# Kernel optimization log

Hardware: AMD Instinct MI355X
Metric: run time of the kernel (lower is better)

Reference implementation:

```python
import jax, jax.numpy as jnp
import numpy as np

B = 262144      # points per batch
DIM = 3         # input_dim
L = 16          # levels
T = 19          # log2 hash table size
F = 2           # features per level
N_MIN, N_MAX = 16, 512

_b = np.exp((np.log(N_MAX) - np.log(N_MIN)) / (L - 1))
RES = np.floor(N_MIN * _b ** np.arange(L)).astype(np.float32).reshape(1, 1, L, 1)

# voxel corner offsets [1, DIM, 1, 2^DIM]
_border = np.empty((DIM, 2 ** DIM), dtype=np.uint32)
for i in range(DIM):
    _border[i, :] = np.array(([0] * 2 ** i + [1] * 2 ** i) * 2 ** (DIM - i - 1), dtype=np.uint32)
BORDER = _border.reshape(1, DIM, 1, 2 ** DIM)

# tiny-cuda-nn hash primes; all fit in uint32. Since the torch code takes the
# result mod 2^T (a power of two), int64 and uint32 arithmetic agree on the
# low bits, so uint32 hashing is bit-exact with the original.
PRIMES = np.array([1, 2654435761, 805459861], dtype=np.uint32)
MASK = np.uint32(2 ** T - 1)


def setup_inputs() -> dict:
    key = jax.random.key(0)
    k1, k2 = jax.random.split(key)
    x = jax.random.uniform(k1, (B, DIM), dtype=jnp.float32)  # coords in [0,1)
    tables = jax.random.uniform(k2, (L, 2 ** T, F), dtype=jnp.float32,
                                minval=-1e-4, maxval=1e-4)
    return {"x": x, "tables": tables}


def reference(x, tables):
    res = jnp.asarray(RES)                                   # [1,1,L,1]
    border = jnp.asarray(BORDER)                             # [1,DIM,1,2^DIM]
    primes = jnp.asarray(PRIMES)
    scaled = x[:, :, None, None] * res                       # [B,DIM,L,1]
    grid = jnp.floor(scaled).astype(jnp.uint32) + border     # [B,DIM,L,2^DIM]
    # spatial hash: xor of per-dim coord * prime, mod 2^T
    h = (grid[:, 0] * primes[0]) ^ (grid[:, 1] * primes[1]) ^ (grid[:, 2] * primes[2])
    idx = (h & MASK).astype(jnp.int32)                       # [B,L,2^DIM]
    gathered = tables[jnp.arange(L)[None, :, None], idx]     # [B,L,2^DIM,F]
    # multilinear interpolation weights
    w = jnp.prod(1.0 - jnp.abs(scaled - grid.astype(scaled.dtype)), axis=1)  # [B,L,2^DIM]
    out = jnp.einsum('blv,blvf->blf', w, gathered)           # [B,L,F]
    return out.reshape(x.shape[0], L * F)
```

## Files before the change

kernel.cpp:

```cpp
#include <hip/hip_runtime.h>


#define NB 262144
#define NL 16
#define TSIZE (1u << 19)
#define TMASK ((1u << 19) - 1u)
#define P1 2654435761u
#define P2 805459861u

#define NCL 3
#define CPTS 8192
#define COARSE_BLOCKS 256
#define CLDS_ENT (17 * 17 * 17)

#define E3 33
#define E4 41
#define E5 51
#define E6 65
#define DOFF3 0
#define DOFF4 35944
#define DOFF5 104872
#define DOFF6 237528
#define DENSE_TOTAL 512160

#define FC1 18513
#define FC2 53814
#define FC3 121440
#define FTOTAL 260865

#define FINE_TOTAL 6656
#define FINE_MAXPX 1024
#define GRID_BLOCKS (COARSE_BLOCKS + 8 * FINE_MAXPX)

typedef float vf2 __attribute__((ext_vector_type(2)));
typedef float vf4 __attribute__((ext_vector_type(4)));
typedef vf4 vf4a8 __attribute__((aligned(8), may_alias));
typedef float vf3 __attribute__((ext_vector_type(3)));
typedef vf3 vf3a4 __attribute__((aligned(4), may_alias));

__constant__ float RES_C[NL] = {16.f, 20.f, 25.f, 32.f, 40.f, 50.f, 64.f, 80.f,
                                101.f, 128.f, 161.f, 203.f, 256.f, 322.f, 406.f, 512.f};

__constant__ int XSPLIT[9] = {0, 1024, 2048, 2816, 3584, 4352, 5120, 5888, 6656};

__device__ __forceinline__ vf3 load_xyz(const float* __restrict__ p) {
  return *(const vf3a4*)p;
}

__device__ __forceinline__ void ngp_point_level(
    float px, float py, float pz, int l, const float* __restrict__ tables,
    float& o0, float& o1) {
  const float res = RES_C[l];
  const float sx = px * res, sy = py * res, sz = pz * res;
  const float fx = floorf(sx), fy = floorf(sy), fz = floorf(sz);
  const unsigned ix = (unsigned)fx, iy = (unsigned)fy, iz = (unsigned)fz;

  const unsigned hy0 = iy * P1, hy1 = hy0 + P1;
  const unsigned hz0 = iz * P2, hz1 = hz0 + P2;

  const float wx0 = 1.0f - fabsf(sx - fx);
  const float wx1 = 1.0f - fabsf(sx - (fx + 1.0f));
  const float wy0 = 1.0f - fabsf(sy - fy);
  const float wy1 = 1.0f - fabsf(sy - (fy + 1.0f));
  const float wz0 = 1.0f - fabsf(sz - fz);
  const float wz1 = 1.0f - fabsf(sz - (fz + 1.0f));

  const vf2* __restrict__ tbl2 = (const vf2*)tables + (size_t)l * TSIZE;
  const vf4* __restrict__ tbl4 = (const vf4*)tables + (size_t)l * (TSIZE / 2);

  unsigned hyz[4];
  hyz[0] = hy0 ^ hz0;
  hyz[1] = hy1 ^ hz0;
  hyz[2] = hy0 ^ hz1;
  hyz[3] = hy1 ^ hz1;

  vf2 g[8];
  if ((ix & 1u) == 0u) {
#pragma unroll
    for (int p = 0; p < 4; ++p) {
      const unsigned i0 = (ix ^ hyz[p]) & TMASK;
      const vf4 q = tbl4[i0 >> 1];
      vf2 lo; lo.x = q.x; lo.y = q.y;
      vf2 hi; hi.x = q.z; hi.y = q.w;
      const bool x0_is_lo = (i0 & 1u) == 0u;
      g[2 * p + 0] = x0_is_lo ? lo : hi;
      g[2 * p + 1] = x0_is_lo ? hi : lo;
    }
  } else {
#pragma unroll
    for (int p = 0; p < 4; ++p) {
      const unsigned i0 = (ix ^ hyz[p]) & TMASK;
      const unsigned i1 = ((ix + 1u) ^ hyz[p]) & TMASK;
      g[2 * p + 0] = tbl2[i0];
      g[2 * p + 1] = tbl2[i1];
    }
  }

  o0 = 0.0f; o1 = 0.0f;
#pragma unroll
  for (int v = 0; v < 8; ++v) {
    const float w = ((v & 1) ? wx1 : wx0) * ((v & 2) ? wy1 : wy0) * ((v & 4) ? wz1 : wz0);
    o0 = fmaf(w, g[v].x, o0);
    o1 = fmaf(w, g[v].y, o1);
  }
}

template <int E, int DOFF_>
__device__ __forceinline__ void dense_point(
    float px, float py, float pz, float res, const vf2* __restrict__ dense,
    float& o0, float& o1) {
  const float sx = px * res, sy = py * res, sz = pz * res;
  const float fx = floorf(sx), fy = floorf(sy), fz = floorf(sz);
  const int ix = (int)fx, iy = (int)fy, iz = (int)fz;

  const float wx0 = 1.0f - fabsf(sx - fx);
  const float wx1 = 1.0f - fabsf(sx - (fx + 1.0f));
  const float wy0 = 1.0f - fabsf(sy - fy);
  const float wy1 = 1.0f - fabsf(sy - (fy + 1.0f));
  const float wz0 = 1.0f - fabsf(sz - fz);
  const float wz1 = 1.0f - fabsf(sz - (fz + 1.0f));

  const vf2* __restrict__ dp = dense + DOFF_ + ix + E * iy + E * E * iz;

  vf2 g[8];
#pragma unroll
  for (int p = 0; p < 4; ++p) {
    const int row = ((p & 1) ? E : 0) + ((p & 2) ? E * E : 0);
    const vf4 q = *(const vf4a8*)(dp + row);
    g[2 * p + 0].x = q.x; g[2 * p + 0].y = q.y;
    g[2 * p + 1].x = q.z; g[2 * p + 1].y = q.w;
  }

  o0 = 0.0f; o1 = 0.0f;
#pragma unroll
  for (int v = 0; v < 8; ++v) {
    const float w = ((v & 1) ? wx1 : wx0) * ((v & 2) ? wy1 : wy0) * ((v & 4) ? wz1 : wz0);
    o0 = fmaf(w, g[v].x, o0);
    o1 = fmaf(w, g[v].y, o1);
  }
}

template <int E, int PLANES>
__device__ __forceinline__ void coarse_slab(
    const int lvl, const int zbase, const int c_lo, const int c_hi,
    const int cchunk, const float* __restrict__ x,
    const float* __restrict__ tables, vf2* __restrict__ ws,
    vf2* __restrict__ cache) {
  const int tid = threadIdx.x;
  const vf4* __restrict__ tbl4 = (const vf4*)tables + (size_t)lvl * (TSIZE / 2);

  constexpr int HE = (E + 1) / 2;
  constexpr int U = HE * E * PLANES;

  for (int u = tid; u < U; u += 512) {
    const int zp = u / (HE * E);
    const int rem = u - zp * (HE * E);
    const int iy = rem / HE;
    const int ixh = rem - iy * HE;
    const unsigned ix = 2u * (unsigned)ixh;
    const unsigned iz = (unsigned)(zbase + zp);
    const unsigned h0 = (ix ^ ((unsigned)iy * P1) ^ (iz * P2)) & TMASK;
    const vf4 q = tbl4[h0 >> 1];
    vf2 lo; lo.x = q.x; lo.y = q.y;
    vf2 hi; hi.x = q.z; hi.y = q.w;
    const bool x0_is_lo = (h0 & 1u) == 0u;
    const int d0 = (int)ix + E * iy + E * E * zp;
    cache[d0] = x0_is_lo ? lo : hi;
    if ((int)ix + 1 < E) cache[d0 + 1] = x0_is_lo ? hi : lo;
  }
  __syncthreads();

  const float res = RES_C[lvl];
  const int base = cchunk * CPTS;
#pragma unroll
  for (int k = 0; k < CPTS / 512; ++k) {
    const int b = base + k * 512 + tid;
    const vf3 pt = load_xyz(x + b * 3);
    const float px = pt.x, py = pt.y, pz = pt.z;

    const float sx = px * res, sy = py * res, sz = pz * res;
    const float fx = floorf(sx), fy = floorf(sy), fz = floorf(sz);
    const int ix = (int)fx, iy = (int)fy, iz = (int)fz;

    if (iz >= c_lo && iz <= c_hi) {
      const float wx0 = 1.0f - fabsf(sx - fx);
      const float wx1 = 1.0f - fabsf(sx - (fx + 1.0f));
      const float wy0 = 1.0f - fabsf(sy - fy);
      const float wy1 = 1.0f - fabsf(sy - (fy + 1.0f));
      const float wz0 = 1.0f - fabsf(sz - fz);
      const float wz1 = 1.0f - fabsf(sz - (fz + 1.0f));

      const int d = ix + E * iy + E * E * (iz - zbase);
      vf2 g[8];
      g[0] = cache[d];
      g[1] = cache[d + 1];
      g[2] = cache[d + E];
      g[3] = cache[d + E + 1];
      g[4] = cache[d + E * E];
      g[5] = cache[d + E * E + 1];
      g[6] = cache[d + E * E + E];
      g[7] = cache[d + E * E + E + 1];

      float o0 = 0.0f, o1 = 0.0f;
#pragma unroll
      for (int v = 0; v < 8; ++v) {
        const float w = ((v & 1) ? wx1 : wx0) * ((v & 2) ? wy1 : wy0) * ((v & 4) ? wz1 : wz0);
        o0 = fmaf(w, g[v].x, o0);
        o1 = fmaf(w, g[v].y, o1);
      }
      vf2 r; r.x = o0; r.y = o1;
      __builtin_nontemporal_store(r, ws + (size_t)lvl * NB + b);
    }
  }
}

__global__ __launch_bounds__(512) void ngp_fill_dense(
    const float* __restrict__ tables, vf2* __restrict__ dense) {
  for (int u = blockIdx.x * 512 + threadIdx.x; u < FTOTAL;
       u += gridDim.x * 512) {
    int lv, E, doff, ubase;
    if (u < FC1)      { lv = 0; E = E3; doff = DOFF3; ubase = 0; }
    else if (u < FC2) { lv = 1; E = E4; doff = DOFF4; ubase = FC1; }
    else if (u < FC3) { lv = 2; E = E5; doff = DOFF5; ubase = FC2; }
    else              { lv = 3; E = E6; doff = DOFF6; ubase = FC3; }
    const int ul = u - ubase;
    const int HE = (E + 1) >> 1;
    const int plane = HE * E;
    const int iz = ul / plane;
    const int rem = ul - iz * plane;
    const int iy = rem / HE;
    const int ixh = rem - iy * HE;
    const unsigned ix = 2u * (unsigned)ixh;
    const unsigned h0 = (ix ^ ((unsigned)iy * P1) ^ ((unsigned)iz * P2)) & TMASK;
    const vf4* __restrict__ tbl4 =
        (const vf4*)tables + (size_t)(NCL + lv) * (TSIZE / 2);
    const vf4 q = tbl4[h0 >> 1];
    vf2 lo; lo.x = q.x; lo.y = q.y;
    vf2 hi; hi.x = q.z; hi.y = q.w;
    const bool el = (h0 & 1u) == 0u;
    const int d0 = doff + (int)ix + E * iy + E * E * iz;
    dense[d0] = el ? lo : hi;
    if ((int)ix + 1 < E) dense[d0 + 1] = el ? hi : lo;
  }
}

__global__ __launch_bounds__(512, 8) void ngp_gather4(
    const float* __restrict__ x, const float* __restrict__ tables,
    vf2* __restrict__ ws) {
  __shared__ vf2 cache[CLDS_ENT];

  const int bid = blockIdx.x;
  if (bid < COARSE_BLOCKS) {
    if (bid < 32) {
      coarse_slab<17, 17>(0, 0, 0, 15, bid, x, tables, ws, cache);
    } else if (bid < 96) {
      const int u = bid - 32;
      const int half = u >> 5;
      coarse_slab<21, 11>(1, half * 10, half * 10, half * 10 + 9, u & 31,
                          x, tables, ws, cache);
    } else {
      const int u = bid - 96;
      const int s = u >> 5;
      coarse_slab<26, 6>(2, 5 * s, 5 * s, 5 * s + 4, u & 31,
                         x, tables, ws, cache);
    }
    return;
  }

  const int fid = bid - COARSE_BLOCKS;
  const int x8 = fid & 7;
  const int j = fid >> 3;
  const int c0 = XSPLIT[x8];
  if (j >= XSPLIT[x8 + 1] - c0) return;
  const int c = c0 + j;
  const int lvl = NCL + (c >> 9);
  const int b = (c & 511) * 512 + threadIdx.x;

  const vf3 pt = load_xyz(x + b * 3);
  const float px = pt.x, py = pt.y, pz = pt.z;

  const vf2* __restrict__ dense = ws + (size_t)NL * NB;

  float o0, o1;
  if (lvl < 7) {
    switch (lvl) {
      case 3:  dense_point<E3, DOFF3>(px, py, pz, RES_C[3], dense, o0, o1); break;
      case 4:  dense_point<E4, DOFF4>(px, py, pz, RES_C[4], dense, o0, o1); break;
      case 5:  dense_point<E5, DOFF5>(px, py, pz, RES_C[5], dense, o0, o1); break;
      default: dense_point<E6, DOFF6>(px, py, pz, RES_C[6], dense, o0, o1); break;
    }
  } else {
    ngp_point_level(px, py, pz, lvl, tables, o0, o1);
  }

  vf2 r; r.x = o0; r.y = o1;
  __builtin_nontemporal_store(r, ws + (size_t)lvl * NB + b);
}

#define FINE_PER_XCD (FINE_TOTAL / 8)
__global__ __launch_bounds__(512, 8) void ngp_gather3(
    const float* __restrict__ x, const float* __restrict__ tables,
    vf2* __restrict__ ws) {
  __shared__ vf2 cache[CLDS_ENT];

  const int bid = blockIdx.x;
  if (bid < COARSE_BLOCKS) {
    if (bid < 32) {
      coarse_slab<17, 17>(0, 0, 0, 15, bid, x, tables, ws, cache);
    } else if (bid < 96) {
      const int u = bid - 32;
      const int half = u >> 5;
      coarse_slab<21, 11>(1, half * 10, half * 10, half * 10 + 9, u & 31,
                          x, tables, ws, cache);
    } else {
      const int u = bid - 96;
      const int s = u >> 5;
      coarse_slab<26, 6>(2, 5 * s, 5 * s, 5 * s + 4, u & 31,
                         x, tables, ws, cache);
    }
    return;
  }

  const int fid = bid - COARSE_BLOCKS;
  const int x8 = fid & 7;
  const int j = fid >> 3;
  const int g = x8 * FINE_PER_XCD + j;
  const int lvl = NCL + (g >> 9);
  const int b = (g & 511) * 512 + threadIdx.x;

  const vf3 pt = load_xyz(x + b * 3);

  float o0, o1;
  ngp_point_level(pt.x, pt.y, pt.z, lvl, tables, o0, o1);

  vf2 r; r.x = o0; r.y = o1;
  __builtin_nontemporal_store(r, ws + (size_t)lvl * NB + b);
}

__global__ __launch_bounds__(256) void ngp_transpose_kernel(
    const vf2* __restrict__ ws, vf4* __restrict__ out4) {
  __shared__ vf2 tile[NL][257];
  const int t = threadIdx.x;
  const int p0 = blockIdx.x * 256;

#pragma unroll
  for (int l = 0; l < NL; ++l) {
    tile[l][t] = __builtin_nontemporal_load(ws + (size_t)l * NB + p0 + t);
  }
  __syncthreads();

#pragma unroll
  for (int k = 0; k < 8; ++k) {
    const int q = k * 256 + t;
    const int pq = q >> 3;
    const int wq = q & 7;
    const vf2 a = tile[2 * wq + 0][pq];
    const vf2 c = tile[2 * wq + 1][pq];
    vf4 v; v.x = a.x; v.y = a.y; v.z = c.x; v.w = c.y;
    __builtin_nontemporal_store(v, out4 + (size_t)p0 * 8 + q);
  }
}

__global__ __launch_bounds__(256) void ngp_fused_kernel(
    const float* __restrict__ x, const float* __restrict__ tables,
    float* __restrict__ out) {
  const int tid = blockIdx.x * blockDim.x + threadIdx.x;
  const int l = tid & (NL - 1);
  const int b = tid >> 4;
  const vf3 pt = load_xyz(x + b * 3);
  float o0, o1;
  ngp_point_level(pt.x, pt.y, pt.z, l, tables, o0, o1);
  float2 r = make_float2(o0, o1);
  ((float2*)out)[tid] = r;
}

extern "C" void kernel_launch(void* const* d_in, const int* in_sizes, int n_in,
                              void* d_out, int out_size, void* d_ws, size_t ws_size,
                              hipStream_t stream) {
  const float* x = (const float*)d_in[0];
  const float* tables = (const float*)d_in[1];
  float* out = (float*)d_out;

  const size_t ws_basic = (size_t)NL * NB * sizeof(vf2);
  const size_t ws_dense = ws_basic + (size_t)DENSE_TOTAL * 8;

  if (ws_size >= ws_dense) {
    vf2* ws = (vf2*)d_ws;
    vf2* dense = ws + (size_t)NL * NB;
    ngp_fill_dense<<<512, 512, 0, stream>>>(tables, dense);
    ngp_gather4<<<GRID_BLOCKS, 512, 0, stream>>>(x, tables, ws);
    ngp_transpose_kernel<<<NB / 256, 256, 0, stream>>>(ws, (vf4*)out);
  } else if (ws_size >= ws_basic) {
    vf2* ws = (vf2*)d_ws;
    ngp_gather3<<<COARSE_BLOCKS + FINE_TOTAL, 512, 0, stream>>>(x, tables, ws);
    ngp_transpose_kernel<<<NB / 256, 256, 0, stream>>>(ws, (vf4*)out);
  } else {
    ngp_fused_kernel<<<NB * NL / 256, 256, 0, stream>>>(x, tables, out);
  }
}
```

Before: 181.8 us.

## Store dense grids as 2x2x2 bricks and densify level 7 too

Dense pre-expanded levels now use a 2x2x2 brick layout, so the 8 corners of a voxel tend to sit in one or few cache lines instead of four separate rows. When the workspace is large enough, level 7 is also densified (81^3 grid), which swaps hashed table gathers for dense brick reads at the cost of a larger fill kernel. The per-XCD work split tables are rebalanced for each tier. Corner loads become eight scalar vf2 loads instead of four vf4 loads, which may add instructions.

```diff
diff --git a/kernel.cpp b/kernel.cpp
--- a/kernel.cpp
+++ b/kernel.cpp
@@ -17,31 +17,33 @@
 #define E4 41
 #define E5 51
 #define E6 65
-#define DOFF3 0
-#define DOFF4 35944
-#define DOFF5 104872
-#define DOFF6 237528
-#define DENSE_TOTAL 512160
+#define E7 81
+#define DB3 0
+#define DB4 39304
+#define DB5 113392
+#define DB6 254000
+#define DB7 541496
+#define DENSE_B 541496
+#define DENSE_A 1092864
 
 #define FC1 18513
 #define FC2 53814
 #define FC3 121440
-#define FTOTAL 260865
+#define FC4 260865
+#define FTOT_A 529866
 
 #define FINE_TOTAL 6656
-#define FINE_MAXPX 1024
-#define GRID_BLOCKS (COARSE_BLOCKS + 8 * FINE_MAXPX)
 
 typedef float vf2 __attribute__((ext_vector_type(2)));
 typedef float vf4 __attribute__((ext_vector_type(4)));
-typedef vf4 vf4a8 __attribute__((aligned(8), may_alias));
 typedef float vf3 __attribute__((ext_vector_type(3)));
 typedef vf3 vf3a4 __attribute__((aligned(4), may_alias));
 
 __constant__ float RES_C[NL] = {16.f, 20.f, 25.f, 32.f, 40.f, 50.f, 64.f, 80.f,
                                 101.f, 128.f, 161.f, 203.f, 256.f, 322.f, 406.f, 512.f};
 
-__constant__ int XSPLIT[9] = {0, 1024, 2048, 2816, 3584, 4352, 5120, 5888, 6656};
+__constant__ int XSPLIT_A[9] = {0, 1192, 2384, 3156, 3856, 4556, 5256, 5956, 6656};
+__constant__ int XSPLIT_B[9] = {0, 1237, 2298, 3024, 3751, 4477, 5203, 5930, 6656};
 
 __device__ __forceinline__ vf3 load_xyz(const float* __restrict__ p) {
   return *(const vf3a4*)p;
@@ -106,9 +108,10 @@
 }
 
 template <int E, int DOFF_>
-__device__ __forceinline__ void dense_point(
+__device__ __forceinline__ void dense_point_brick(
     float px, float py, float pz, float res, const vf2* __restrict__ dense,
     float& o0, float& o1) {
+  constexpr int BD = (E + 1) / 2;
   const float sx = px * res, sy = py * res, sz = pz * res;
   const float fx = floorf(sx), fy = floorf(sy), fz = floorf(sz);
   const int ix = (int)fx, iy = (int)fy, iz = (int)fz;
@@ -120,16 +123,28 @@
   const float wz0 = 1.0f - fabsf(sz - fz);
   const float wz1 = 1.0f - fabsf(sz - (fz + 1.0f));
 
-  const vf2* __restrict__ dp = dense + DOFF_ + ix + E * iy + E * E * iz;
-
+  const int bx0 = ix >> 1, ox0 = ix & 1;
+  const int bx1 = (ix + 1) >> 1, ox1 = (ix + 1) & 1;
+  const int by0 = iy >> 1, oy0 = (iy & 1) * 2;
+  const int by1 = (iy + 1) >> 1, oy1 = ((iy + 1) & 1) * 2;
+  const int bz0 = iz >> 1, oz0 = (iz & 1) * 4;
+  const int bz1 = (iz + 1) >> 1, oz1 = ((iz + 1) & 1) * 4;
+
+  const int r00 = ((bz0 * BD + by0) * BD) * 8;
+  const int r10 = ((bz0 * BD + by1) * BD) * 8;
+  const int r01 = ((bz1 * BD + by0) * BD) * 8;
+  const int r11 = ((bz1 * BD + by1) * BD) * 8;
+
+  const vf2* __restrict__ d = dense + DOFF_;
   vf2 g[8];
-#pragma unroll
-  for (int p = 0; p < 4; ++p) {
-    const int row = ((p & 1) ? E : 0) + ((p & 2) ? E * E : 0);
-    const vf4 q = *(const vf4a8*)(dp + row);
-    g[2 * p + 0].x = q.x; g[2 * p + 0].y = q.y;
-    g[2 * p + 1].x = q.z; g[2 * p + 1].y = q.w;
-  }
+  g[0] = d[r00 + bx0 * 8 + oz0 + oy0 + ox0];
+  g[1] = d[r00 + bx1 * 8 + oz0 + oy0 + ox1];
+  g[2] = d[r10 + bx0 * 8 + oz0 + oy1 + ox0];
+  g[3] = d[r10 + bx1 * 8 + oz0 + oy1 + ox1];
+  g[4] = d[r01 + bx0 * 8 + oz1 + oy0 + ox0];
+  g[5] = d[r01 + bx1 * 8 + oz1 + oy0 + ox1];
+  g[6] = d[r11 + bx0 * 8 + oz1 + oy1 + ox0];
+  g[7] = d[r11 + bx1 * 8 + oz1 + oy1 + ox1];
 
   o0 = 0.0f; o1 = 0.0f;
 #pragma unroll
@@ -214,22 +229,24 @@
   }
 }
 
+template <bool WITH_L7>
 __global__ __launch_bounds__(512) void ngp_fill_dense(
     const float* __restrict__ tables, vf2* __restrict__ dense) {
-  for (int u = blockIdx.x * 512 + threadIdx.x; u < FTOTAL;
+  const int ftotal = WITH_L7 ? FTOT_A : FC4;
+  for (int u = blockIdx.x * 512 + threadIdx.x; u < ftotal;
        u += gridDim.x * 512) {
-    int lv, E, doff, ubase;
-    if (u < FC1)      { lv = 0; E = E3; doff = DOFF3; ubase = 0; }
-    else if (u < FC2) { lv = 1; E = E4; doff = DOFF4; ubase = FC1; }
-    else if (u < FC3) { lv = 2; E = E5; doff = DOFF5; ubase = FC2; }
-    else              { lv = 3; E = E6; doff = DOFF6; ubase = FC3; }
+    int lv, E, BD, doff, ubase;
+    if (u < FC1)      { lv = 0; E = E3; BD = 17; doff = DB3; ubase = 0; }
+    else if (u < FC2) { lv = 1; E = E4; BD = 21; doff = DB4; ubase = FC1; }
+    else if (u < FC3) { lv = 2; E = E5; BD = 26; doff = DB5; ubase = FC2; }
+    else if (u < FC4) { lv = 3; E = E6; BD = 33; doff = DB6; ubase = FC3; }
+    else              { lv = 4; E = E7; BD = 41; doff = DB7; ubase = FC4; }
     const int ul = u - ubase;
-    const int HE = (E + 1) >> 1;
-    const int plane = HE * E;
+    const int plane = BD * E;
     const int iz = ul / plane;
     const int rem = ul - iz * plane;
-    const int iy = rem / HE;
-    const int ixh = rem - iy * HE;
+    const int iy = rem / BD;
+    const int ixh = rem - iy * BD;
     const unsigned ix = 2u * (unsigned)ixh;
     const unsigned h0 = (ix ^ ((unsigned)iy * P1) ^ ((unsigned)iz * P2)) & TMASK;
     const vf4* __restrict__ tbl4 =
@@ -238,13 +255,17 @@
     vf2 lo; lo.x = q.x; lo.y = q.y;
     vf2 hi; hi.x = q.z; hi.y = q.w;
     const bool el = (h0 & 1u) == 0u;
-    const int d0 = doff + (int)ix + E * iy + E * E * iz;
-    dense[d0] = el ? lo : hi;
-    if ((int)ix + 1 < E) dense[d0 + 1] = el ? hi : lo;
-  }
-}
-
-__global__ __launch_bounds__(512, 8) void ngp_gather4(
+    const int brick = ((iz >> 1) * BD + (iy >> 1)) * BD + (int)(ix >> 1);
+    const int ent = doff + brick * 8 + (iz & 1) * 4 + (iy & 1) * 2;
+    vf4 w;
+    if (el) { w.x = lo.x; w.y = lo.y; w.z = hi.x; w.w = hi.y; }
+    else    { w.x = hi.x; w.y = hi.y; w.z = lo.x; w.w = lo.y; }
+    *(vf4*)(dense + ent) = w;
+  }
+}
+
+template <int TIER>
+__global__ __launch_bounds__(512, 8) void ngp_gather5(
     const float* __restrict__ x, const float* __restrict__ tables,
     vf2* __restrict__ ws) {
   __shared__ vf2 cache[CLDS_ENT];
@@ -267,11 +288,12 @@
     return;
   }
 
+  const int* xs = (TIER == 0) ? XSPLIT_A : XSPLIT_B;
   const int fid = bid - COARSE_BLOCKS;
   const int x8 = fid & 7;
   const int j = fid >> 3;
-  const int c0 = XSPLIT[x8];
-  if (j >= XSPLIT[x8 + 1] - c0) return;
+  const int c0 = xs[x8];
+  if (j >= xs[x8 + 1] - c0) return;
   const int c = c0 + j;
   const int lvl = NCL + (c >> 9);
   const int b = (c & 511) * 512 + threadIdx.x;
@@ -280,14 +302,16 @@
   const float px = pt.x, py = pt.y, pz = pt.z;
 
   const vf2* __restrict__ dense = ws + (size_t)NL * NB;
+  const int dcut = (TIER == 0) ? 8 : 7;
 
   float o0, o1;
-  if (lvl < 7) {
+  if (lvl < dcut) {
     switch (lvl) {
-      case 3:  dense_point<E3, DOFF3>(px, py, pz, RES_C[3], dense, o0, o1); break;
-      case 4:  dense_point<E4, DOFF4>(px, py, pz, RES_C[4], dense, o0, o1); break;
-      case 5:  dense_point<E5, DOFF5>(px, py, pz, RES_C[5], dense, o0, o1); break;
-      default: dense_point<E6, DOFF6>(px, py, pz, RES_C[6], dense, o0, o1); break;
+      case 3:  dense_point_brick<E3, DB3>(px, py, pz, RES_C[3], dense, o0, o1); break;
+      case 4:  dense_point_brick<E4, DB4>(px, py, pz, RES_C[4], dense, o0, o1); break;
+      case 5:  dense_point_brick<E5, DB5>(px, py, pz, RES_C[5], dense, o0, o1); break;
+      case 6:  dense_point_brick<E6, DB6>(px, py, pz, RES_C[6], dense, o0, o1); break;
+      default: dense_point_brick<E7, DB7>(px, py, pz, RES_C[7], dense, o0, o1); break;
     }
   } else {
     ngp_point_level(px, py, pz, lvl, tables, o0, o1);
@@ -382,13 +406,20 @@
   float* out = (float*)d_out;
 
   const size_t ws_basic = (size_t)NL * NB * sizeof(vf2);
-  const size_t ws_dense = ws_basic + (size_t)DENSE_TOTAL * 8;
-
-  if (ws_size >= ws_dense) {
+  const size_t ws_tierB = ws_basic + (size_t)DENSE_B * 8;
+  const size_t ws_tierA = ws_basic + (size_t)DENSE_A * 8;
+
+  if (ws_size >= ws_tierA) {
     vf2* ws = (vf2*)d_ws;
     vf2* dense = ws + (size_t)NL * NB;
-    ngp_fill_dense<<<512, 512, 0, stream>>>(tables, dense);
-    ngp_gather4<<<GRID_BLOCKS, 512, 0, stream>>>(x, tables, ws);
+    ngp_fill_dense<true><<<1024, 512, 0, stream>>>(tables, dense);
+    ngp_gather5<0><<<COARSE_BLOCKS + 8 * 1192, 512, 0, stream>>>(x, tables, ws);
+    ngp_transpose_kernel<<<NB / 256, 256, 0, stream>>>(ws, (vf4*)out);
+  } else if (ws_size >= ws_tierB) {
+    vf2* ws = (vf2*)d_ws;
+    vf2* dense = ws + (size_t)NL * NB;
+    ngp_fill_dense<false><<<512, 512, 0, stream>>>(tables, dense);
+    ngp_gather5<1><<<COARSE_BLOCKS + 8 * 1237, 512, 0, stream>>>(x, tables, ws);
     ngp_transpose_kernel<<<NB / 256, 256, 0, stream>>>(ws, (vf4*)out);
   } else if (ws_size >= ws_basic) {
     vf2* ws = (vf2*)d_ws;
```

Result: slower. 221.4 us (+21.8%).
